# Kernel tuning notes

Hardware: AMD Instinct MI355X
Metric: run time of the kernel (lower is better)

Reference implementation:

```python
import jax, jax.numpy as jnp
import numpy as np

B, T, C = 64, 4096, 256
H = 4
HD = C // H  # head_dim = 64
EPS = 1e-5   # torch LayerNorm default


def setup_inputs() -> dict:
    key = jax.random.key(0)
    ks = jax.random.split(key, 8)
    x = jax.random.normal(ks[0], (B, T, C), dtype=jnp.float32)
    # per-head score MLP: Linear(C->HD) + Tanh + Linear(HD->1, no bias)
    W1 = jax.random.normal(ks[1], (H, C, HD), dtype=jnp.float32) * (1.0 / np.sqrt(C))
    b1 = jax.random.normal(ks[2], (H, HD), dtype=jnp.float32) * 0.02
    w2 = jax.random.normal(ks[3], (H, HD), dtype=jnp.float32) * (1.0 / np.sqrt(HD))
    # output projection Linear(H*C -> C), torch layout (out, in)
    Wo = jax.random.normal(ks[4], (C, H * C), dtype=jnp.float32) * (1.0 / np.sqrt(H * C))
    bo = jax.random.normal(ks[5], (C,), dtype=jnp.float32) * 0.02
    gamma = jnp.ones((C,), dtype=jnp.float32)
    beta = jnp.zeros((C,), dtype=jnp.float32)
    return {"x": x, "W1": W1, "b1": b1, "w2": w2, "Wo": Wo, "bo": bo,
            "gamma": gamma, "beta": beta}


def reference(x, W1, b1, w2, Wo, bo, gamma, beta):
    # All heads batched: hidden (B,H,T,HD)
    h = jnp.tanh(jnp.einsum('btc,hcd->bhtd', x, W1) + b1[None, :, None, :])
    scores = jnp.einsum('bhtd,hd->bht', h, w2)            # (B,H,T)
    weights = jax.nn.softmax(scores, axis=-1)             # softmax over T
    contexts = jnp.einsum('bht,btc->bhc', weights, x)     # (B,H,C)
    multi = contexts.reshape(B, H * C)                    # concat over heads
    out = multi @ Wo.T + bo                               # Linear(H*C->C)
    # LayerNorm over last dim (dropout is identity in eval mode)
    mu = jnp.mean(out, axis=-1, keepdims=True)
    var = jnp.mean(jnp.square(out - mu), axis=-1, keepdims=True)
    out = (out - mu) * jax.lax.rsqrt(var + EPS) * gamma + beta
    return out, weights
```

## Files before the change

kernel.cpp:

```cpp
#include <hip/hip_runtime.h>
#include <hip/hip_bf16.h>
#include <math.h>

#define B_ 64
#define T_ 4096
#define C_ 256
#define H_ 4
#define HD_ 64
#define EPS_ 1e-5f

typedef __attribute__((ext_vector_type(4))) float floatx4;
typedef __attribute__((ext_vector_type(8))) short short8;

__device__ __forceinline__ unsigned int pack_bf16x2(float a, float b) {
    unsigned int ua = __builtin_bit_cast(unsigned int, a);
    unsigned int ub = __builtin_bit_cast(unsigned int, b);
    ua = (ua + 0x7fffu + ((ua >> 16) & 1u)) >> 16;
    ub = (ub + 0x7fffu + ((ub >> 16) & 1u)) >> 16;
    return ua | (ub << 16);
}

__global__ void k0_w1t(const float* __restrict__ W1, unsigned short* __restrict__ w1t) {
    int n = blockIdx.x;
    int c = threadIdx.x;
    int h = n >> 6, d = n & 63;
    float v = W1[(h * C_ + c) * HD_ + d];
    unsigned int u = __builtin_bit_cast(unsigned int, v);
    u = (u + 0x7fffu + ((u >> 16) & 1u)) >> 16;
    w1t[n * C_ + c] = (unsigned short)u;
}

__global__ __launch_bounds__(256, 3)
void k1_fused(const float* __restrict__ x, const unsigned short* __restrict__ w1t,
              const float* __restrict__ b1, const float* __restrict__ w2,
              float* __restrict__ rawscore, float* __restrict__ ctxp,
              float* __restrict__ mS) {
    __shared__ __align__(16) unsigned short shA[64 * 40];
    __shared__ __align__(16) unsigned short shB[256 * 40];
    __shared__ float sS[4 * 64];
    __shared__ float sP[4 * 64];

    const int tid  = threadIdx.x;
    const int lane = tid & 63;
    const int w    = tid >> 6;
    const int nl   = lane & 15;
    const int q    = lane >> 4;
    const int rowbase = blockIdx.x * 64;
    const int b       = blockIdx.x >> 6;
    const int tbase   = (blockIdx.x & 63) * 64;

    floatx4 acc[4][4];
    #pragma unroll
    for (int i = 0; i < 4; ++i)
        #pragma unroll
        for (int j = 0; j < 4; ++j)
            acc[i][j] = (floatx4){0.f, 0.f, 0.f, 0.f};

    const int arow = tid >> 2;
    const int acol = (tid & 3) * 8;
    const float* aptr = x + (long)(rowbase + arow) * C_ + acol;
    const unsigned short* bptr = w1t + tid * C_;

    float4 fa0 = ((const float4*)aptr)[0];
    float4 fa1 = ((const float4*)aptr)[1];
    uint4  fb0 = ((const uint4*)bptr)[0];
    uint4  fb1 = ((const uint4*)bptr)[1];
    uint4  fb2 = ((const uint4*)bptr)[2];
    uint4  fb3 = ((const uint4*)bptr)[3];

    for (int ks = 0; ks < 8; ++ks) {
        uint4 ua;
        ua.x = pack_bf16x2(fa0.x, fa0.y); ua.y = pack_bf16x2(fa0.z, fa0.w);
        ua.z = pack_bf16x2(fa1.x, fa1.y); ua.w = pack_bf16x2(fa1.z, fa1.w);
        *(uint4*)&shA[arow * 40 + acol] = ua;
        uint4* bd = (uint4*)&shB[tid * 40];
        bd[0] = fb0; bd[1] = fb1; bd[2] = fb2; bd[3] = fb3;
        __syncthreads();
        if (ks < 7) {
            const float4* ap = (const float4*)(aptr + (ks + 1) * 32);
            fa0 = ap[0]; fa1 = ap[1];
            const uint4* bp = (const uint4*)(bptr + (ks + 1) * 32);
            fb0 = bp[0]; fb1 = bp[1]; fb2 = bp[2]; fb3 = bp[3];
        }
        short8 aF[4], bF[4];
        #pragma unroll
        for (int mb = 0; mb < 4; ++mb)
            aF[mb] = *(const short8*)&shA[(mb * 16 + nl) * 40 + q * 8];
        #pragma unroll
        for (int nb = 0; nb < 4; ++nb)
            bF[nb] = *(const short8*)&shB[(w * 64 + nb * 16 + nl) * 40 + q * 8];
        #pragma unroll
        for (int mb = 0; mb < 4; ++mb)
            #pragma unroll
            for (int nb = 0; nb < 4; ++nb)
                acc[mb][nb] = __builtin_amdgcn_mfma_f32_16x16x32_bf16(
                    aF[mb], bF[nb], acc[mb][nb], 0, 0, 0);
        __syncthreads();
    }

    float b1v[4], w2v[4];
    #pragma unroll
    for (int nb = 0; nb < 4; ++nb) {
        int d = nb * 16 + nl;
        b1v[nb] = b1[w * HD_ + d];
        w2v[nb] = w2[w * HD_ + d];
    }
    #pragma unroll
    for (int mb = 0; mb < 4; ++mb) {
        float p[4];
        #pragma unroll
        for (int r = 0; r < 4; ++r) {
            float s = 0.f;
            #pragma unroll
            for (int nb = 0; nb < 4; ++nb)
                s += tanhf(acc[mb][nb][r] + b1v[nb]) * w2v[nb];
            p[r] = s;
        }
        #pragma unroll
        for (int m = 1; m < 16; m <<= 1)
            #pragma unroll
            for (int r = 0; r < 4; ++r)
                p[r] += __shfl_xor(p[r], m, 64);
        if (nl == 0) {
            #pragma unroll
            for (int r = 0; r < 4; ++r)
                sS[w * 64 + mb * 16 + q * 4 + r] = p[r];
        }
    }

    {
        float s = sS[w * 64 + lane];
        float m = s;
        #pragma unroll
        for (int off = 1; off < 64; off <<= 1)
            m = fmaxf(m, __shfl_xor(m, off, 64));
        float e = expf(s - m);
        float Ss = e;
        #pragma unroll
        for (int off = 1; off < 64; off <<= 1)
            Ss += __shfl_xor(Ss, off, 64);
        sP[w * 64 + lane] = e;
        rawscore[((long)(b * H_ + w)) * T_ + tbase + lane] = s;
        if (lane == 0) {
            mS[((long)blockIdx.x * H_ + w) * 2 + 0] = m;
            mS[((long)blockIdx.x * H_ + w) * 2 + 1] = Ss;
        }
    }
    __syncthreads();

    {
        float c0 = 0.f, c1 = 0.f, c2 = 0.f, c3 = 0.f;
        const float* xr = x + (long)rowbase * C_ + tid;
        #pragma unroll 8
        for (int t = 0; t < 64; ++t) {
            float xv = xr[(long)t * C_];
            c0 += sP[t] * xv;
            c1 += sP[64 + t] * xv;
            c2 += sP[128 + t] * xv;
            c3 += sP[192 + t] * xv;
        }
        float* o = ctxp + (long)blockIdx.x * (H_ * C_) + tid;
        o[0]   = c0;
        o[256] = c1;
        o[512] = c2;
        o[768] = c3;
    }
}

__global__ void k2_combine(const float* __restrict__ ctxp, const float* __restrict__ mS,
                           float* __restrict__ weights, float* __restrict__ multi) {
    __shared__ float sm[64], sSl[64], sc[64];
    int bh = blockIdx.x;
    int b = bh >> 2, h = bh & 3;
    int tid = threadIdx.x;
    if (tid < 64) {
        long blk = (long)b * 64 + tid;
        sm[tid]  = mS[(blk * H_ + h) * 2 + 0];
        sSl[tid] = mS[(blk * H_ + h) * 2 + 1];
    }
    __syncthreads();
    float m = -INFINITY;
    #pragma unroll 8
    for (int j = 0; j < 64; ++j) m = fmaxf(m, sm[j]);
    if (tid < 64) sc[tid] = expf(sm[tid] - m);
    __syncthreads();
    float S = 0.f;
    #pragma unroll 8
    for (int j = 0; j < 64; ++j) S += sSl[j] * sc[j];
    float invS = 1.0f / S;

    float acc = 0.f;
    #pragma unroll 4
    for (int j = 0; j < 64; ++j)
        acc += ctxp[((long)(b * 64 + j) * H_ + h) * C_ + tid] * sc[j];
    multi[(long)b * (H_ * C_) + h * C_ + tid] = acc * invS;

    float* wr = weights + (long)bh * T_;
    #pragma unroll
    for (int i = 0; i < 16; ++i) {
        int t = tid + i * 256;
        float sv = wr[t];
        wr[t] = expf(sv - m) * invS;
    }
}

__global__ void k4_out(const float* __restrict__ multiG, const float* __restrict__ Wo,
                       const float* __restrict__ bo, const float* __restrict__ gamma,
                       const float* __restrict__ beta, float* __restrict__ out) {
    __shared__ float multi[1024];
    __shared__ float red[256];
    int b = blockIdx.x, tid = threadIdx.x;
    #pragma unroll
    for (int j = 0; j < 4; ++j) {
        int idx = tid + j * 256;
        multi[idx] = multiG[(long)b * 1024 + idx];
    }
    __syncthreads();
    float acc = bo[tid];
    const float4* wrow = (const float4*)(Wo + (long)tid * 1024);
    #pragma unroll 4
    for (int j4 = 0; j4 < 256; ++j4) {
        float4 wv = wrow[j4];
        acc += multi[j4 * 4] * wv.x + multi[j4 * 4 + 1] * wv.y +
               multi[j4 * 4 + 2] * wv.z + multi[j4 * 4 + 3] * wv.w;
    }
    red[tid] = acc; __syncthreads();
    for (int st = 128; st > 0; st >>= 1) {
        if (tid < st) red[tid] += red[tid + st];
        __syncthreads();
    }
    float mu = red[0] * (1.0f / 256.0f); __syncthreads();
    float dv = acc - mu;
    red[tid] = dv * dv; __syncthreads();
    for (int st = 128; st > 0; st >>= 1) {
        if (tid < st) red[tid] += red[tid + st];
        __syncthreads();
    }
    float var = red[0] * (1.0f / 256.0f);
    out[(long)b * C_ + tid] = dv * rsqrtf(var + EPS_) * gamma[tid] + beta[tid];
}

extern "C" void kernel_launch(void* const* d_in, const int* in_sizes, int n_in,
                              void* d_out, int out_size, void* d_ws, size_t ws_size,
                              hipStream_t stream) {
    const float* x     = (const float*)d_in[0];
    const float* W1    = (const float*)d_in[1];
    const float* b1    = (const float*)d_in[2];
    const float* w2    = (const float*)d_in[3];
    const float* Wo    = (const float*)d_in[4];
    const float* bo    = (const float*)d_in[5];
    const float* gamma = (const float*)d_in[6];
    const float* beta  = (const float*)d_in[7];

    float* out     = (float*)d_out;
    float* weights = out + B_ * C_;

    float* ctxp  = (float*)d_ws;
    float* mS    = ctxp + (long)4096 * H_ * C_;
    float* multi = mS + (long)4096 * H_ * 2;
    unsigned short* w1t = (unsigned short*)(multi + B_ * H_ * C_);

    k0_w1t    <<<256, 256, 0, stream>>>(W1, w1t);
    k1_fused  <<<4096, 256, 0, stream>>>(x, w1t, b1, w2, weights, ctxp, mS);
    k2_combine<<<256, 256, 0, stream>>>(ctxp, mS, weights, multi);
    k4_out    <<<64, 256, 0, stream>>>(multi, Wo, bo, gamma, beta, out);
}
```

Measured before the change: 487.2 us.

## Load MFMA fragments directly from global, use fast tanh/exp, vectorize reductions

```diff
diff --git a/kernel.cpp b/kernel.cpp
--- a/kernel.cpp
+++ b/kernel.cpp
@@ -12,12 +12,27 @@
 typedef __attribute__((ext_vector_type(4))) float floatx4;
 typedef __attribute__((ext_vector_type(8))) short short8;
 
+#if __has_builtin(__builtin_amdgcn_cvt_pk_bf16_f32)
+typedef __attribute__((ext_vector_type(2))) __bf16 bf16x2_t;
+__device__ __forceinline__ unsigned int pack_bf16x2(float a, float b) {
+    bf16x2_t v = __builtin_amdgcn_cvt_pk_bf16_f32(a, b);
+    return __builtin_bit_cast(unsigned int, v);
+}
+#else
 __device__ __forceinline__ unsigned int pack_bf16x2(float a, float b) {
     unsigned int ua = __builtin_bit_cast(unsigned int, a);
     unsigned int ub = __builtin_bit_cast(unsigned int, b);
     ua = (ua + 0x7fffu + ((ua >> 16) & 1u)) >> 16;
     ub = (ub + 0x7fffu + ((ub >> 16) & 1u)) >> 16;
     return ua | (ub << 16);
+}
+#endif
+
+__device__ __forceinline__ float fast_tanh(float v) {
+    float a = fabsf(v);
+    float e = __expf(-2.0f * a);
+    float r = (1.0f - e) / (1.0f + e);
+    return copysignf(r, v);
 }
 
 __global__ void k0_w1t(const float* __restrict__ W1, unsigned short* __restrict__ w1t) {
@@ -35,10 +50,8 @@
               const float* __restrict__ b1, const float* __restrict__ w2,
               float* __restrict__ rawscore, float* __restrict__ ctxp,
               float* __restrict__ mS) {
-    __shared__ __align__(16) unsigned short shA[64 * 40];
-    __shared__ __align__(16) unsigned short shB[256 * 40];
     __shared__ float sS[4 * 64];
-    __shared__ float sP[4 * 64];
+    __shared__ __align__(16) float sP4[64 * 4];
 
     const int tid  = threadIdx.x;
     const int lane = tid & 63;
@@ -56,46 +69,30 @@
         for (int j = 0; j < 4; ++j)
             acc[i][j] = (floatx4){0.f, 0.f, 0.f, 0.f};
 
-    const int arow = tid >> 2;
-    const int acol = (tid & 3) * 8;
-    const float* aptr = x + (long)(rowbase + arow) * C_ + acol;
-    const unsigned short* bptr = w1t + tid * C_;
-
-    float4 fa0 = ((const float4*)aptr)[0];
-    float4 fa1 = ((const float4*)aptr)[1];
-    uint4  fb0 = ((const uint4*)bptr)[0];
-    uint4  fb1 = ((const uint4*)bptr)[1];
-    uint4  fb2 = ((const uint4*)bptr)[2];
-    uint4  fb3 = ((const uint4*)bptr)[3];
+    const float* aBase = x + (long)(rowbase + nl) * C_ + q * 8;
+    const unsigned short* bBase = w1t + (long)(w * 64 + nl) * C_ + q * 8;
 
     for (int ks = 0; ks < 8; ++ks) {
-        uint4 ua;
-        ua.x = pack_bf16x2(fa0.x, fa0.y); ua.y = pack_bf16x2(fa0.z, fa0.w);
-        ua.z = pack_bf16x2(fa1.x, fa1.y); ua.w = pack_bf16x2(fa1.z, fa1.w);
-        *(uint4*)&shA[arow * 40 + acol] = ua;
-        uint4* bd = (uint4*)&shB[tid * 40];
-        bd[0] = fb0; bd[1] = fb1; bd[2] = fb2; bd[3] = fb3;
-        __syncthreads();
-        if (ks < 7) {
-            const float4* ap = (const float4*)(aptr + (ks + 1) * 32);
-            fa0 = ap[0]; fa1 = ap[1];
-            const uint4* bp = (const uint4*)(bptr + (ks + 1) * 32);
-            fb0 = bp[0]; fb1 = bp[1]; fb2 = bp[2]; fb3 = bp[3];
-        }
-        short8 aF[4], bF[4];
-        #pragma unroll
-        for (int mb = 0; mb < 4; ++mb)
-            aF[mb] = *(const short8*)&shA[(mb * 16 + nl) * 40 + q * 8];
+        const int kb = ks * 32;
+        uint4 bF[4];
         #pragma unroll
         for (int nb = 0; nb < 4; ++nb)
-            bF[nb] = *(const short8*)&shB[(w * 64 + nb * 16 + nl) * 40 + q * 8];
-        #pragma unroll
-        for (int mb = 0; mb < 4; ++mb)
+            bF[nb] = *(const uint4*)(bBase + nb * 16 * C_ + kb);
+        #pragma unroll
+        for (int mb = 0; mb < 4; ++mb) {
+            const float4* ap = (const float4*)(aBase + (long)mb * 16 * C_ + kb);
+            float4 f0 = ap[0], f1 = ap[1];
+            uint4 ua;
+            ua.x = pack_bf16x2(f0.x, f0.y);
+            ua.y = pack_bf16x2(f0.z, f0.w);
+            ua.z = pack_bf16x2(f1.x, f1.y);
+            ua.w = pack_bf16x2(f1.z, f1.w);
+            short8 aF = __builtin_bit_cast(short8, ua);
             #pragma unroll
             for (int nb = 0; nb < 4; ++nb)
                 acc[mb][nb] = __builtin_amdgcn_mfma_f32_16x16x32_bf16(
-                    aF[mb], bF[nb], acc[mb][nb], 0, 0, 0);
-        __syncthreads();
+                    aF, __builtin_bit_cast(short8, bF[nb]), acc[mb][nb], 0, 0, 0);
+        }
     }
 
     float b1v[4], w2v[4];
@@ -113,7 +110,7 @@
             float s = 0.f;
             #pragma unroll
             for (int nb = 0; nb < 4; ++nb)
-                s += tanhf(acc[mb][nb][r] + b1v[nb]) * w2v[nb];
+                s += fast_tanh(acc[mb][nb][r] + b1v[nb]) * w2v[nb];
             p[r] = s;
         }
         #pragma unroll
@@ -134,12 +131,12 @@
         #pragma unroll
         for (int off = 1; off < 64; off <<= 1)
             m = fmaxf(m, __shfl_xor(m, off, 64));
-        float e = expf(s - m);
+        float e = __expf(s - m);
         float Ss = e;
         #pragma unroll
         for (int off = 1; off < 64; off <<= 1)
             Ss += __shfl_xor(Ss, off, 64);
-        sP[w * 64 + lane] = e;
+        sP4[lane * 4 + w] = e;
         rawscore[((long)(b * H_ + w)) * T_ + tbase + lane] = s;
         if (lane == 0) {
             mS[((long)blockIdx.x * H_ + w) * 2 + 0] = m;
@@ -151,13 +148,15 @@
     {
         float c0 = 0.f, c1 = 0.f, c2 = 0.f, c3 = 0.f;
         const float* xr = x + (long)rowbase * C_ + tid;
+        const float4* pv4 = (const float4*)sP4;
         #pragma unroll 8
         for (int t = 0; t < 64; ++t) {
             float xv = xr[(long)t * C_];
-            c0 += sP[t] * xv;
-            c1 += sP[64 + t] * xv;
-            c2 += sP[128 + t] * xv;
-            c3 += sP[192 + t] * xv;
+            float4 pv = pv4[t];
+            c0 += pv.x * xv;
+            c1 += pv.y * xv;
+            c2 += pv.z * xv;
+            c3 += pv.w * xv;
         }
         float* o = ctxp + (long)blockIdx.x * (H_ * C_) + tid;
         o[0]   = c0;
@@ -182,7 +181,7 @@
     float m = -INFINITY;
     #pragma unroll 8
     for (int j = 0; j < 64; ++j) m = fmaxf(m, sm[j]);
-    if (tid < 64) sc[tid] = expf(sm[tid] - m);
+    if (tid < 64) sc[tid] = __expf(sm[tid] - m);
     __syncthreads();
     float S = 0.f;
     #pragma unroll 8
@@ -200,7 +199,7 @@
     for (int i = 0; i < 16; ++i) {
         int t = tid + i * 256;
         float sv = wr[t];
-        wr[t] = expf(sv - m) * invS;
+        wr[t] = __expf(sv - m) * invS;
     }
 }
 
@@ -210,20 +209,27 @@
     __shared__ float multi[1024];
     __shared__ float red[256];
     int b = blockIdx.x, tid = threadIdx.x;
-    #pragma unroll
-    for (int j = 0; j < 4; ++j) {
-        int idx = tid + j * 256;
-        multi[idx] = multiG[(long)b * 1024 + idx];
-    }
-    __syncthreads();
-    float acc = bo[tid];
+    {
+        const float4* src = (const float4*)(multiG + (long)b * 1024);
+        float4* dst = (float4*)multi;
+        if (tid < 256) dst[tid] = src[tid];
+    }
+    __syncthreads();
+    float a0 = 0.f, a1 = 0.f, a2 = 0.f, a3 = 0.f;
     const float4* wrow = (const float4*)(Wo + (long)tid * 1024);
-    #pragma unroll 4
-    for (int j4 = 0; j4 < 256; ++j4) {
-        float4 wv = wrow[j4];
-        acc += multi[j4 * 4] * wv.x + multi[j4 * 4 + 1] * wv.y +
-               multi[j4 * 4 + 2] * wv.z + multi[j4 * 4 + 3] * wv.w;
-    }
+    const float4* mv = (const float4*)multi;
+    #pragma unroll 8
+    for (int j4 = 0; j4 < 256; j4 += 4) {
+        float4 w0 = wrow[j4],     m0 = mv[j4];
+        float4 w1 = wrow[j4 + 1], m1 = mv[j4 + 1];
+        float4 w2 = wrow[j4 + 2], m2 = mv[j4 + 2];
+        float4 w3 = wrow[j4 + 3], m3 = mv[j4 + 3];
+        a0 += m0.x * w0.x + m0.y * w0.y + m0.z * w0.z + m0.w * w0.w;
+        a1 += m1.x * w1.x + m1.y * w1.y + m1.z * w1.z + m1.w * w1.w;
+        a2 += m2.x * w2.x + m2.y * w2.y + m2.z * w2.z + m2.w * w2.w;
+        a3 += m3.x * w3.x + m3.y * w3.y + m3.z * w3.z + m3.w * w3.w;
+    }
+    float acc = bo[tid] + ((a0 + a1) + (a2 + a3));
     red[tid] = acc; __syncthreads();
     for (int st = 128; st > 0; st >>= 1) {
         if (tid < st) red[tid] += red[tid + st];
```

After: 574.5 us. +17.9%, slower.
